# Optimization experiments

Measured on AMD Instinct MI355X. Metric: run time of the kernel, lower is better.

The kernel has to match this reference:

```python
import jax, jax.numpy as jnp
import numpy as np

B, L, IN, H, P, K, OUT = 16, 4096, 192, 512, 128, 6, 192  # P = ssm_size//2 (conj_sym)


def setup_inputs() -> dict:
    key = jax.random.key(0)
    ks = jax.random.split(key, 20)
    s = 1.0 / np.sqrt(H)
    inp = {
        'x': jax.random.normal(ks[0], (B, L, IN), jnp.float32),
        'W_enc': jax.random.normal(ks[1], (H, IN), jnp.float32) / np.sqrt(IN),
        'b_enc': jnp.zeros((H,), jnp.float32),
        'ln_scale': jnp.ones((K, H), jnp.float32),
        'ln_bias': jnp.zeros((K, H), jnp.float32),
        # HiPPO-like stable eigenvalues: negative real part
        'Lambda_re': -(0.5 * jax.random.uniform(ks[2], (K, P), jnp.float32) + 0.1),
        'Lambda_im': jnp.pi * jax.random.normal(ks[3], (K, P), jnp.float32),
        'B_re': jax.random.normal(ks[4], (K, P, H), jnp.float32) * s,
        'B_im': jax.random.normal(ks[5], (K, P, H), jnp.float32) * s,
        'C_re': jax.random.normal(ks[6], (K, H, P), jnp.float32) / np.sqrt(P),
        'C_im': jax.random.normal(ks[7], (K, H, P), jnp.float32) / np.sqrt(P),
        'D': jax.random.normal(ks[8], (K, H), jnp.float32),
        'log_step': jax.random.uniform(ks[9], (K, P), jnp.float32,
                                       minval=np.log(1e-3), maxval=np.log(1e-1)),
        'W_glu': jax.random.normal(ks[10], (K, H, H), jnp.float32) * s,
        'b_glu': jnp.zeros((K, H), jnp.float32),
        'W_dec': jax.random.normal(ks[11], (OUT, H), jnp.float32) * s,
        'b_dec': jnp.zeros((OUT,), jnp.float32),
    }
    return inp


def _layernorm(x, scale, bias, eps=1e-5):
    mu = jnp.mean(x, axis=-1, keepdims=True)
    var = jnp.var(x, axis=-1, keepdims=True)
    return (x - mu) * jax.lax.rsqrt(var + eps) * scale + bias


def _s5_ssm(u, lam_re, lam_im, b_re, b_im, c_re, c_im, d, log_step):
    # u: (L, H) real. Diagonal complex SSM, ZOH discretization, conj_sym output.
    lam = lam_re + 1j * lam_im                     # (P,)
    step = jnp.exp(log_step)                       # (P,) step_rescale = 1
    lam_bar = jnp.exp(lam * step)                  # (P,)
    Bm = b_re + 1j * b_im                          # (P, H)
    B_bar = ((lam_bar - 1.0) / lam)[:, None] * Bm  # ZOH input matrix
    Bu = u.astype(B_bar.dtype) @ B_bar.T           # (L, P) complex
    A = jnp.broadcast_to(lam_bar, Bu.shape)        # (L, P)

    def binop(e1, e2):
        a1, x1 = e1
        a2, x2 = e2
        return a2 * a1, a2 * x1 + x2

    _, xs = jax.lax.associative_scan(binop, (A, Bu))  # linear recurrence over L
    Cm = c_re + 1j * c_im                          # (H, P)
    y = 2.0 * jnp.real(xs @ Cm.T)                  # factor 2 from conjugate symmetry
    return y + u * d


def reference(x, W_enc, b_enc, ln_scale, ln_bias, Lambda_re, Lambda_im,
              B_re, B_im, C_re, C_im, D, log_step, W_glu, b_glu, W_dec, b_dec):
    def fwd_seq(xs):  # xs: (L, IN)
        h = xs @ W_enc.T + b_enc                   # encoder, vmapped over time
        for k in range(K):                         # stacked S5 blocks (prenorm)
            skip = h
            h = _layernorm(h, ln_scale[k], ln_bias[k])
            h = _s5_ssm(h, Lambda_re[k], Lambda_im[k], B_re[k], B_im[k],
                        C_re[k], C_im[k], D[k], log_step[k])
            h = jax.nn.gelu(h)
            h = h * jax.nn.sigmoid(h @ W_glu[k].T + b_glu[k])  # half-GLU
            h = skip + h
        return h @ W_dec.T + b_dec                 # decoder

    return jax.vmap(fwd_seq)(x)
```

## Files before the change

kernel.cpp:

```cpp
#include <hip/hip_runtime.h>
#include <math.h>

constexpr int  Bb   = 16;
constexpr int  Ll   = 4096;
constexpr int  INd  = 192;
constexpr int  Hd   = 512;
constexpr int  Kn   = 6;
constexpr int  OUTd = 192;
constexpr long Mrows = (long)Bb * Ll;

typedef _Float16 f16;
typedef _Float16 f16x8 __attribute__((ext_vector_type(8)));
typedef float    f32x4 __attribute__((ext_vector_type(4)));

__global__ void prep_lam_k(const float* __restrict__ Lre, const float* __restrict__ Lim,
                           const float* __restrict__ lstep,
                           float* lre, float* lim_, float* pre, float* pim,
                           float* cre, float* cim)
{
    int i = blockIdx.x * 256 + threadIdx.x;
    if (i >= Kn * 128) return;
    float lr = Lre[i], li = Lim[i];
    float st = expf(lstep[i]);
    float ar = lr * st, ai = li * st;
    float er = expf(ar);
    float sn, cs; sincosf(ai, &sn, &cs);
    float br = er * cs, bi = er * sn;
    lre[i] = br; lim_[i] = bi;
    float e2 = expf(64.f * ar);
    float sn2, cs2; sincosf(64.f * ai, &sn2, &cs2);
    pre[i] = e2 * cs2; pim[i] = e2 * sn2;
    float nr = br - 1.f, ni = bi;
    float den = lr * lr + li * li;
    cre[i] = (nr * lr + ni * li) / den;
    cim[i] = (ni * lr - nr * li) / den;
}

__global__ void prep_bbar_k(const float* __restrict__ Bre, const float* __restrict__ Bim,
                            const float* __restrict__ cre, const float* __restrict__ cim,
                            f16* __restrict__ Wh)
{
    int i = blockIdx.x * 256 + threadIdx.x;
    int h = i & 511;
    int p = (i >> 9) & 127;
    int k = i >> 16;
    float br = Bre[((size_t)(k * 128 + p)) * 512 + h];
    float bi = Bim[((size_t)(k * 128 + p)) * 512 + h];
    float cr = cre[k * 128 + p], ci = cim[k * 128 + p];
    Wh[(size_t)(k * 256 + p) * 512 + h]       = (f16)(cr * br - ci * bi);
    Wh[(size_t)(k * 256 + 128 + p) * 512 + h] = (f16)(cr * bi + ci * br);
}

__global__ void prep_c_k(const float* __restrict__ Cre, const float* __restrict__ Cim,
                         f16* __restrict__ Wh)
{
    int i = blockIdx.x * 256 + threadIdx.x;
    int p = i & 127;
    int h = (i >> 7) & 511;
    int k = i >> 16;
    float crv = Cre[((size_t)k * 512 + h) * 128 + p];
    float civ = Cim[((size_t)k * 512 + h) * 128 + p];
    size_t o = ((size_t)k * 512 + h) * 256;
    Wh[o + p]       = (f16)( 2.f * crv);
    Wh[o + 128 + p] = (f16)(-2.f * civ);
}

__global__ void cvt_w_k(const float* __restrict__ W, f16* __restrict__ Wh, long n)
{
    long i = (long)blockIdx.x * 256 + threadIdx.x;
    if (i >= n) return;
    Wh[i] = (f16)W[i];
}

__global__ __launch_bounds__(256)
void cvt_a_k(const float* __restrict__ in, f16* __restrict__ oh, long n8)
{
    long i = (long)blockIdx.x * 256 + threadIdx.x;
    if (i >= n8) return;
    const float* p = in + i * 8;
    float v[8];
    *(float4*)&v[0] = *(const float4*)p;
    *(float4*)&v[4] = *(const float4*)(p + 4);
    f16x8 vh;
#pragma unroll
    for (int j = 0; j < 8; ++j) vh[j] = (f16)v[j];
    *(f16x8*)(oh + i * 8) = vh;
}

__global__ __launch_bounds__(256)
void ln_k(const float* __restrict__ x, f16* __restrict__ oh,
          const float* __restrict__ sc, const float* __restrict__ bi)
{
    const int  lane = threadIdx.x & 63;
    const long row  = (long)blockIdx.x * 4 + (threadIdx.x >> 6);
    const float* p = x + row * 512 + lane * 8;
    float v[8];
    *(float4*)&v[0] = *(const float4*)p;
    *(float4*)&v[4] = *(const float4*)(p + 4);
    float s = 0.f;
#pragma unroll
    for (int j = 0; j < 8; ++j) s += v[j];
#pragma unroll
    for (int m = 1; m < 64; m <<= 1) s += __shfl_xor(s, m, 64);
    const float mu = s * (1.f / 512.f);
    float q = 0.f;
#pragma unroll
    for (int j = 0; j < 8; ++j) { float d = v[j] - mu; q += d * d; }
#pragma unroll
    for (int m = 1; m < 64; m <<= 1) q += __shfl_xor(q, m, 64);
    const float rs = rsqrtf(q * (1.f / 512.f) + 1e-5f);
    float sv[8], bv[8];
    *(float4*)&sv[0] = *(const float4*)(sc + lane * 8);
    *(float4*)&sv[4] = *(const float4*)(sc + lane * 8 + 4);
    *(float4*)&bv[0] = *(const float4*)(bi + lane * 8);
    *(float4*)&bv[4] = *(const float4*)(bi + lane * 8 + 4);
    f16x8 vh;
#pragma unroll
    for (int j = 0; j < 8; ++j)
        vh[j] = (f16)((v[j] - mu) * rs * sv[j] + bv[j]);
    *(f16x8*)(oh + row * 512 + lane * 8) = vh;
}

__global__ __launch_bounds__(256)
void scan_local_k(const float* __restrict__ Bu, float* __restrict__ fin,
                  const float* __restrict__ lre, const float* __restrict__ lim, int nB)
{
    const int g = blockIdx.x * 256 + threadIdx.x;
    const int p = g & 127;
    const int c = (g >> 7) & 63;
    const int b = g >> 13;
    if (b >= nB) return;
    const float ar = lre[p], ai = lim[p];
    const float* base = Bu + ((long)(b * Ll + c * 64)) * 256 + p;
    float xr = 0.f, xi = 0.f;
#pragma unroll 4
    for (int j = 0; j < 64; ++j) {
        float br  = base[j * 256];
        float bi2 = base[j * 256 + 128];
        float nr = fmaf(ar, xr, fmaf(-ai, xi, br));
        float ni = fmaf(ar, xi, fmaf( ai, xr, bi2));
        xr = nr; xi = ni;
    }
    long o = ((long)(b * 64 + c)) * 256 + p;
    fin[o] = xr; fin[o + 128] = xi;
}

__global__ void scan_carry_k(const float* __restrict__ fin, float* __restrict__ carry,
                             const float* __restrict__ pre, const float* __restrict__ pim,
                             int nB)
{
    const int g = blockIdx.x * 256 + threadIdx.x;
    if (g >= nB * 128) return;
    const int p = g & 127;
    const int b = g >> 7;
    const float pr = pre[p], pi = pim[p];
    float cr = 0.f, ci = 0.f;
    for (int c = 0; c < 64; ++c) {
        long o = ((long)(b * 64 + c)) * 256 + p;
        float fr = fin[o], fi = fin[o + 128];
        carry[o] = cr; carry[o + 128] = ci;
        float nr = fmaf(pr, cr, fmaf(-pi, ci, fr));
        float ni = fmaf(pr, ci, fmaf( pi, cr, fi));
        cr = nr; ci = ni;
    }
}

__global__ __launch_bounds__(256)
void scan_final_k(const float* __restrict__ Bu, const float* __restrict__ carry,
                  f16* __restrict__ xh,
                  const float* __restrict__ lre, const float* __restrict__ lim, int nB)
{
    const int g = blockIdx.x * 256 + threadIdx.x;
    const int p = g & 127;
    const int c = (g >> 7) & 63;
    const int b = g >> 13;
    if (b >= nB) return;
    const float ar = lre[p], ai = lim[p];
    long co = ((long)(b * 64 + c)) * 256 + p;
    float xr = carry[co], xi = carry[co + 128];
    const float* base = Bu + ((long)(b * Ll + c * 64)) * 256 + p;
    f16* bh = xh + ((long)(b * Ll + c * 64)) * 256 + p;
#pragma unroll 4
    for (int j = 0; j < 64; ++j) {
        float br  = base[j * 256];
        float bi2 = base[j * 256 + 128];
        float nr = fmaf(ar, xr, fmaf(-ai, xi, br));
        float ni = fmaf(ar, xi, fmaf( ai, xr, bi2));
        xr = nr; xi = ni;
        bh[j * 256]       = (f16)xr;
        bh[j * 256 + 128] = (f16)xi;
    }
}

template<int BN, int EPI>
__global__ __launch_bounds__(256)
void mgemm_k(const f16* __restrict__ A, const f16* __restrict__ Bw,
             float* __restrict__ C, int N, int Kd,
             const float* __restrict__ bias,
             const f16* __restrict__ aux, f16* __restrict__ outq)
{
    constexpr int BM = 128, BK = 32, LDA = 40;
    constexpr int FM = (BN == 128) ? 4 : 2;
    constexpr int WM = FM * 16;
    constexpr int FN = 4;
    __shared__ __align__(16) f16 As[BM][LDA];
    __shared__ __align__(16) f16 Bs[BN][LDA];

    const int tid  = threadIdx.x;
    const int wid  = tid >> 6;
    const int lane = tid & 63;
    const int l15  = lane & 15;
    const int l4   = lane >> 4;
    const int wm   = (BN == 128) ? (wid >> 1) : wid;
    const int wn   = (BN == 128) ? (wid & 1) : 0;

    const long bm = (long)blockIdx.y * BM;
    const int  bn = blockIdx.x * BN;

    f32x4 acc[FM][FN];
#pragma unroll
    for (int i = 0; i < FM; ++i)
#pragma unroll
        for (int j = 0; j < FN; ++j) acc[i][j] = (f32x4){0.f, 0.f, 0.f, 0.f};

    const int arow = tid >> 1;
    const int akc  = (tid & 1) * 16;
    const int brow = (BN == 128) ? (tid >> 1) : (tid >> 2);
    const int bko  = (BN == 128) ? ((tid & 1) * 16) : ((tid & 3) * 8);
    constexpr int NBL = (BN == 128) ? 2 : 1;

    f16x8 ra[2], rb[2];
    auto LOADT = [&](int k0) {
        const long aoff = (bm + arow) * (long)Kd + k0 + akc;
        ra[0] = *(const f16x8*)(A + aoff);
        ra[1] = *(const f16x8*)(A + aoff + 8);
        const long boff = (long)(bn + brow) * Kd + k0 + bko;
        rb[0] = *(const f16x8*)(Bw + boff);
        if constexpr (NBL == 2) rb[1] = *(const f16x8*)(Bw + boff + 8);
    };

    LOADT(0);
    for (int k0 = 0; k0 < Kd; k0 += BK) {
        __syncthreads();
        *(f16x8*)&As[arow][akc]     = ra[0];
        *(f16x8*)&As[arow][akc + 8] = ra[1];
        *(f16x8*)&Bs[brow][bko] = rb[0];
        if constexpr (NBL == 2) *(f16x8*)&Bs[brow][bko + 8] = rb[1];
        __syncthreads();
        if (k0 + BK < Kd) LOADT(k0 + BK);

        f16x8 bf[FN];
#pragma unroll
        for (int j = 0; j < FN; ++j)
            bf[j] = *(const f16x8*)&Bs[wn * 64 + j * 16 + l15][l4 * 8];
#pragma unroll
        for (int i = 0; i < FM; ++i) {
            f16x8 af = *(const f16x8*)&As[wm * WM + i * 16 + l15][l4 * 8];
#pragma unroll
            for (int j = 0; j < FN; ++j)
                acc[i][j] = __builtin_amdgcn_mfma_f32_16x16x32_f16(af, bf[j], acc[i][j], 0, 0, 0);
        }
    }

#pragma unroll
    for (int i = 0; i < FM; ++i)
#pragma unroll
        for (int j = 0; j < FN; ++j) {
            const int n = bn + wn * 64 + j * 16 + l15;
            float bv = 0.f;
            if constexpr (EPI != 0) bv = bias[n];
#pragma unroll
            for (int r = 0; r < 4; ++r) {
                const long m = bm + wm * WM + i * 16 + l4 * 4 + r;
                const long off = m * N + n;
                float v = acc[i][j][r];
                if constexpr (EPI == 0) {
                    C[off] = v;
                } else if constexpr (EPI == 1) {
                    C[off] = v + bv;
                } else if constexpr (EPI == 2) {
                    float y = v + (float)aux[off] * bv;
                    float t = tanhf(0.7978845608028654f * (y + 0.044715f * y * y * y));
                    outq[off] = (f16)(0.5f * y * (1.f + t));
                } else {
                    float z = v + bv;
                    C[off] += (float)aux[off] / (1.f + expf(-z));
                }
            }
        }
}

extern "C" void kernel_launch(void* const* d_in, const int* in_sizes, int n_in,
                              void* d_out, int out_size, void* d_ws, size_t ws_size,
                              hipStream_t stream)
{
    const float* x        = (const float*)d_in[0];
    const float* W_enc    = (const float*)d_in[1];
    const float* b_enc    = (const float*)d_in[2];
    const float* ln_scale = (const float*)d_in[3];
    const float* ln_bias  = (const float*)d_in[4];
    const float* Lre      = (const float*)d_in[5];
    const float* Lim      = (const float*)d_in[6];
    const float* B_re     = (const float*)d_in[7];
    const float* B_im     = (const float*)d_in[8];
    const float* C_re     = (const float*)d_in[9];
    const float* C_im     = (const float*)d_in[10];
    const float* Dv       = (const float*)d_in[11];
    const float* log_step = (const float*)d_in[12];
    const float* W_glu    = (const float*)d_in[13];
    const float* b_glu    = (const float*)d_in[14];
    const float* W_dec    = (const float*)d_in[15];
    const float* b_dec    = (const float*)d_in[16];
    float* out = (float*)d_out;

    char* w = (char*)d_ws;
    auto alloc = [&](size_t nbytes) { char* p = w; w += (nbytes + 255) & ~255ull; return p; };

    float* lam_re = (float*)alloc(768 * 4);
    float* lam_im = (float*)alloc(768 * 4);
    float* pow_re = (float*)alloc(768 * 4);
    float* pow_im = (float*)alloc(768 * 4);
    float* coef_re= (float*)alloc(768 * 4);
    float* coef_im= (float*)alloc(768 * 4);
    float* fin    = (float*)alloc((size_t)Bb * 64 * 256 * 4);
    float* carry  = (float*)alloc((size_t)Bb * 64 * 256 * 4);
    f16* WencH = (f16*)alloc((size_t)Hd * INd * 2);
    f16* WbuH  = (f16*)alloc((size_t)Kn * 256 * Hd * 2);
    f16* WcH   = (f16*)alloc((size_t)Kn * Hd * 256 * 2);
    f16* WgluH = (f16*)alloc((size_t)Kn * Hd * Hd * 2);
    f16* WdecH = (f16*)alloc((size_t)OUTd * Hd * 2);
    const size_t fixed_bytes = (size_t)(w - (char*)d_ws);

    int G = 1;
    for (; G < 16; G *= 2) {
        size_t Mg = Mrows / G;
        if (fixed_bytes + Mg * 4992ull <= ws_size) break;
    }
    const long Bg = Bb / G;
    const long Mg = Bg * Ll;

    float* h   = (float*)alloc((size_t)Mg * Hd * 4);
    f16*   uh  = (f16*)alloc((size_t)Mg * Hd * 2);
    float* Bu  = (float*)alloc((size_t)Mg * 256 * 4);
    f16*   xsh = (f16*)alloc((size_t)Mg * 256 * 2);
    f16*   xh  = (f16*)alloc((size_t)Mg * INd * 2);

    prep_lam_k <<<3,    256, 0, stream>>>(Lre, Lim, log_step, lam_re, lam_im,
                                          pow_re, pow_im, coef_re, coef_im);
    prep_bbar_k<<<1536, 256, 0, stream>>>(B_re, B_im, coef_re, coef_im, WbuH);
    prep_c_k   <<<1536, 256, 0, stream>>>(C_re, C_im, WcH);
    cvt_w_k    <<<6144, 256, 0, stream>>>(W_glu, WgluH, (long)Kn * Hd * Hd);
    cvt_w_k    <<<384,  256, 0, stream>>>(W_enc, WencH, (long)Hd * INd);
    cvt_w_k    <<<384,  256, 0, stream>>>(W_dec, WdecH, (long)OUTd * Hd);

    const dim3 blk(256);
    const int gy = (int)(Mg / 128);
    for (int g0 = 0; g0 < G; ++g0) {
        const float* xg   = x   + (size_t)g0 * Mg * INd;
        float*       outg = out + (size_t)g0 * Mg * OUTd;

        cvt_a_k<<<(int)(Mg * INd / 2048), 256, 0, stream>>>(xg, xh, Mg * INd / 8);
        mgemm_k<128, 1><<<dim3(4, gy), blk, 0, stream>>>(
            xh, WencH, h, 512, INd, b_enc, nullptr, nullptr);

        for (int k = 0; k < Kn; ++k) {
            ln_k<<<(int)(Mg / 4), 256, 0, stream>>>(h, uh,
                                                    ln_scale + k * 512, ln_bias + k * 512);
            mgemm_k<128, 0><<<dim3(2, gy), blk, 0, stream>>>(
                uh, WbuH + (size_t)k * 256 * Hd, Bu, 256, 512, nullptr, nullptr, nullptr);
            scan_local_k<<<(int)(Bg * 32), 256, 0, stream>>>(
                Bu, fin, lam_re + k * 128, lam_im + k * 128, (int)Bg);
            scan_carry_k<<<(int)((Bg * 128 + 255) / 256), 256, 0, stream>>>(
                fin, carry, pow_re + k * 128, pow_im + k * 128, (int)Bg);
            scan_final_k<<<(int)(Bg * 32), 256, 0, stream>>>(
                Bu, carry, xsh, lam_re + k * 128, lam_im + k * 128, (int)Bg);
            mgemm_k<128, 2><<<dim3(4, gy), blk, 0, stream>>>(
                xsh, WcH + (size_t)k * Hd * 256, nullptr, 512, 256,
                Dv + k * 512, uh, uh);
            mgemm_k<128, 3><<<dim3(4, gy), blk, 0, stream>>>(
                uh, WgluH + (size_t)k * Hd * Hd, h, 512, 512,
                b_glu + k * 512, uh, nullptr);
        }
        cvt_a_k<<<(int)(Mg * Hd / 2048), 256, 0, stream>>>(h, uh, Mg * Hd / 8);
        mgemm_k<64, 1><<<dim3(3, gy), blk, 0, stream>>>(
            uh, WdecH, outg, 192, 512, b_dec, nullptr, nullptr);
    }
}
```

Measured before the change: 2.471 ms.

## Fuse f32-to-f16 conversions into GEMMs, store Bu in fp16, parallelize carry scan

The encoder GEMM now reads fp32 input and converts it while loading, and the final GLU GEMM writes an fp16 copy of h for the decoder, which removes both standalone conversion kernels. Bu is stored as fp16 instead of fp32, halving the traffic for the two scan passes. The carry scan becomes a wave-level parallel prefix scan with shuffles instead of a serial loop over chunks. MFMA operands are swapped so each lane holds four consecutive columns, which lets the epilogues use vectorized 4-wide stores. Storing Bu in fp16 loses precision in the recurrence input.

```diff
diff --git a/kernel.cpp b/kernel.cpp
--- a/kernel.cpp
+++ b/kernel.cpp
@@ -11,6 +11,7 @@
 
 typedef _Float16 f16;
 typedef _Float16 f16x8 __attribute__((ext_vector_type(8)));
+typedef _Float16 f16x4 __attribute__((ext_vector_type(4)));
 typedef float    f32x4 __attribute__((ext_vector_type(4)));
 
 __global__ void prep_lam_k(const float* __restrict__ Lre, const float* __restrict__ Lim,
@@ -73,21 +74,6 @@
 }
 
 __global__ __launch_bounds__(256)
-void cvt_a_k(const float* __restrict__ in, f16* __restrict__ oh, long n8)
-{
-    long i = (long)blockIdx.x * 256 + threadIdx.x;
-    if (i >= n8) return;
-    const float* p = in + i * 8;
-    float v[8];
-    *(float4*)&v[0] = *(const float4*)p;
-    *(float4*)&v[4] = *(const float4*)(p + 4);
-    f16x8 vh;
-#pragma unroll
-    for (int j = 0; j < 8; ++j) vh[j] = (f16)v[j];
-    *(f16x8*)(oh + i * 8) = vh;
-}
-
-__global__ __launch_bounds__(256)
 void ln_k(const float* __restrict__ x, f16* __restrict__ oh,
           const float* __restrict__ sc, const float* __restrict__ bi)
 {
@@ -122,7 +108,7 @@
 }
 
 __global__ __launch_bounds__(256)
-void scan_local_k(const float* __restrict__ Bu, float* __restrict__ fin,
+void scan_local_k(const f16* __restrict__ Bu, float* __restrict__ fin,
                   const float* __restrict__ lre, const float* __restrict__ lim, int nB)
 {
     const int g = blockIdx.x * 256 + threadIdx.x;
@@ -131,12 +117,12 @@
     const int b = g >> 13;
     if (b >= nB) return;
     const float ar = lre[p], ai = lim[p];
-    const float* base = Bu + ((long)(b * Ll + c * 64)) * 256 + p;
+    const f16* base = Bu + ((long)(b * Ll + c * 64)) * 256 + p;
     float xr = 0.f, xi = 0.f;
 #pragma unroll 4
     for (int j = 0; j < 64; ++j) {
-        float br  = base[j * 256];
-        float bi2 = base[j * 256 + 128];
+        float br  = (float)base[j * 256];
+        float bi2 = (float)base[j * 256 + 128];
         float nr = fmaf(ar, xr, fmaf(-ai, xi, br));
         float ni = fmaf(ar, xi, fmaf( ai, xr, bi2));
         xr = nr; xi = ni;
@@ -145,28 +131,40 @@
     fin[o] = xr; fin[o + 128] = xi;
 }
 
-__global__ void scan_carry_k(const float* __restrict__ fin, float* __restrict__ carry,
-                             const float* __restrict__ pre, const float* __restrict__ pim,
-                             int nB)
-{
-    const int g = blockIdx.x * 256 + threadIdx.x;
-    if (g >= nB * 128) return;
-    const int p = g & 127;
-    const int b = g >> 7;
-    const float pr = pre[p], pi = pim[p];
-    float cr = 0.f, ci = 0.f;
-    for (int c = 0; c < 64; ++c) {
-        long o = ((long)(b * 64 + c)) * 256 + p;
-        float fr = fin[o], fi = fin[o + 128];
-        carry[o] = cr; carry[o + 128] = ci;
-        float nr = fmaf(pr, cr, fmaf(-pi, ci, fr));
-        float ni = fmaf(pr, ci, fmaf( pi, cr, fi));
-        cr = nr; ci = ni;
-    }
-}
-
 __global__ __launch_bounds__(256)
-void scan_final_k(const float* __restrict__ Bu, const float* __restrict__ carry,
+void scan_carry_k(const float* __restrict__ fin, float* __restrict__ carry,
+                  const float* __restrict__ pre, const float* __restrict__ pim, int nB)
+{
+    const int wv   = blockIdx.x * 4 + (threadIdx.x >> 6);
+    const int lane = threadIdx.x & 63;
+    if (wv >= nB * 128) return;
+    const int b = wv >> 7;
+    const int p = wv & 127;
+    const long o = ((long)(b * 64 + lane)) * 256 + p;
+    float xr = fin[o], xi = fin[o + 128];
+    float ar = pre[p], ai = pim[p];
+#pragma unroll
+    for (int s = 1; s < 64; s <<= 1) {
+        float par = __shfl_up(ar, s, 64);
+        float pai = __shfl_up(ai, s, 64);
+        float pxr = __shfl_up(xr, s, 64);
+        float pxi = __shfl_up(xi, s, 64);
+        if (lane >= s) {
+            float nxr = fmaf(ar, pxr, fmaf(-ai, pxi, xr));
+            float nxi = fmaf(ar, pxi, fmaf( ai, pxr, xi));
+            float nar = ar * par - ai * pai;
+            float nai = ar * pai + ai * par;
+            xr = nxr; xi = nxi; ar = nar; ai = nai;
+        }
+    }
+    float cr = __shfl_up(xr, 1, 64);
+    float ci = __shfl_up(xi, 1, 64);
+    if (lane == 0) { cr = 0.f; ci = 0.f; }
+    carry[o] = cr; carry[o + 128] = ci;
+}
+
+__global__ __launch_bounds__(256)
+void scan_final_k(const f16* __restrict__ Bu, const float* __restrict__ carry,
                   f16* __restrict__ xh,
                   const float* __restrict__ lre, const float* __restrict__ lim, int nB)
 {
@@ -178,12 +176,12 @@
     const float ar = lre[p], ai = lim[p];
     long co = ((long)(b * 64 + c)) * 256 + p;
     float xr = carry[co], xi = carry[co + 128];
-    const float* base = Bu + ((long)(b * Ll + c * 64)) * 256 + p;
+    const f16* base = Bu + ((long)(b * Ll + c * 64)) * 256 + p;
     f16* bh = xh + ((long)(b * Ll + c * 64)) * 256 + p;
 #pragma unroll 4
     for (int j = 0; j < 64; ++j) {
-        float br  = base[j * 256];
-        float bi2 = base[j * 256 + 128];
+        float br  = (float)base[j * 256];
+        float bi2 = (float)base[j * 256 + 128];
         float nr = fmaf(ar, xr, fmaf(-ai, xi, br));
         float ni = fmaf(ar, xi, fmaf( ai, xr, bi2));
         xr = nr; xi = ni;
@@ -192,9 +190,9 @@
     }
 }
 
-template<int BN, int EPI>
+template<int BN, int EPI, bool AF32>
 __global__ __launch_bounds__(256)
-void mgemm_k(const f16* __restrict__ A, const f16* __restrict__ Bw,
+void mgemm_k(const void* __restrict__ Ap, const f16* __restrict__ Bw,
              float* __restrict__ C, int N, int Kd,
              const float* __restrict__ bias,
              const f16* __restrict__ aux, f16* __restrict__ outq)
@@ -205,6 +203,9 @@
     constexpr int FN = 4;
     __shared__ __align__(16) f16 As[BM][LDA];
     __shared__ __align__(16) f16 Bs[BN][LDA];
+
+    const f16*   A16 = (const f16*)Ap;
+    const float* A32 = (const float*)Ap;
 
     const int tid  = threadIdx.x;
     const int wid  = tid >> 6;
@@ -231,9 +232,21 @@
 
     f16x8 ra[2], rb[2];
     auto LOADT = [&](int k0) {
-        const long aoff = (bm + arow) * (long)Kd + k0 + akc;
-        ra[0] = *(const f16x8*)(A + aoff);
-        ra[1] = *(const f16x8*)(A + aoff + 8);
+        if constexpr (AF32) {
+            const float* ap = A32 + (bm + arow) * (long)Kd + k0 + akc;
+            float4 t0 = ((const float4*)ap)[0];
+            float4 t1 = ((const float4*)ap)[1];
+            float4 t2 = ((const float4*)ap)[2];
+            float4 t3 = ((const float4*)ap)[3];
+            ra[0] = (f16x8){(f16)t0.x,(f16)t0.y,(f16)t0.z,(f16)t0.w,
+                            (f16)t1.x,(f16)t1.y,(f16)t1.z,(f16)t1.w};
+            ra[1] = (f16x8){(f16)t2.x,(f16)t2.y,(f16)t2.z,(f16)t2.w,
+                            (f16)t3.x,(f16)t3.y,(f16)t3.z,(f16)t3.w};
+        } else {
+            const long aoff = (bm + arow) * (long)Kd + k0 + akc;
+            ra[0] = *(const f16x8*)(A16 + aoff);
+            ra[1] = *(const f16x8*)(A16 + aoff + 8);
+        }
         const long boff = (long)(bn + brow) * Kd + k0 + bko;
         rb[0] = *(const f16x8*)(Bw + boff);
         if constexpr (NBL == 2) rb[1] = *(const f16x8*)(Bw + boff + 8);
@@ -258,36 +271,50 @@
             f16x8 af = *(const f16x8*)&As[wm * WM + i * 16 + l15][l4 * 8];
 #pragma unroll
             for (int j = 0; j < FN; ++j)
-                acc[i][j] = __builtin_amdgcn_mfma_f32_16x16x32_f16(af, bf[j], acc[i][j], 0, 0, 0);
+                acc[i][j] = __builtin_amdgcn_mfma_f32_16x16x32_f16(bf[j], af, acc[i][j], 0, 0, 0);
         }
     }
 
 #pragma unroll
-    for (int i = 0; i < FM; ++i)
+    for (int i = 0; i < FM; ++i) {
+        const int m = (int)(bm + wm * WM + i * 16 + l15);
 #pragma unroll
         for (int j = 0; j < FN; ++j) {
-            const int n = bn + wn * 64 + j * 16 + l15;
-            float bv = 0.f;
-            if constexpr (EPI != 0) bv = bias[n];
-#pragma unroll
-            for (int r = 0; r < 4; ++r) {
-                const long m = bm + wm * WM + i * 16 + l4 * 4 + r;
-                const long off = m * N + n;
-                float v = acc[i][j][r];
-                if constexpr (EPI == 0) {
-                    C[off] = v;
-                } else if constexpr (EPI == 1) {
-                    C[off] = v + bv;
-                } else if constexpr (EPI == 2) {
-                    float y = v + (float)aux[off] * bv;
+            const int  n0  = bn + wn * 64 + j * 16 + l4 * 4;
+            const long off = (long)m * N + n0;
+            f32x4 v = acc[i][j];
+            if constexpr (EPI == 0) {
+                *(f16x4*)(outq + off) = (f16x4){(f16)v[0], (f16)v[1], (f16)v[2], (f16)v[3]};
+            } else if constexpr (EPI == 1) {
+                const float4 bb = *(const float4*)(bias + n0);
+                *(float4*)(C + off) = make_float4(v[0]+bb.x, v[1]+bb.y, v[2]+bb.z, v[3]+bb.w);
+            } else if constexpr (EPI == 2) {
+                const float4 bb = *(const float4*)(bias + n0);
+                const f16x4 uu = *(const f16x4*)(aux + off);
+                f16x4 o4;
+#pragma unroll
+                for (int r = 0; r < 4; ++r) {
+                    float bvr = (r == 0 ? bb.x : r == 1 ? bb.y : r == 2 ? bb.z : bb.w);
+                    float y = v[r] + (float)uu[r] * bvr;
                     float t = tanhf(0.7978845608028654f * (y + 0.044715f * y * y * y));
-                    outq[off] = (f16)(0.5f * y * (1.f + t));
-                } else {
-                    float z = v + bv;
-                    C[off] += (float)aux[off] / (1.f + expf(-z));
+                    o4[r] = (f16)(0.5f * y * (1.f + t));
                 }
+                *(f16x4*)(outq + off) = o4;
+            } else {
+                const float4 bb = *(const float4*)(bias + n0);
+                const f16x4 uu = *(const f16x4*)(aux + off);
+                float4 hh = *(const float4*)(C + off);
+                float z0 = v[0]+bb.x, z1 = v[1]+bb.y, z2 = v[2]+bb.z, z3 = v[3]+bb.w;
+                hh.x += (float)uu[0] / (1.f + expf(-z0));
+                hh.y += (float)uu[1] / (1.f + expf(-z1));
+                hh.z += (float)uu[2] / (1.f + expf(-z2));
+                hh.w += (float)uu[3] / (1.f + expf(-z3));
+                *(float4*)(C + off) = hh;
+                if constexpr (EPI == 4)
+                    *(f16x4*)(outq + off) = (f16x4){(f16)hh.x, (f16)hh.y, (f16)hh.z, (f16)hh.w};
             }
         }
+    }
 }
 
 extern "C" void kernel_launch(void* const* d_in, const int* in_sizes, int n_in,
@@ -334,16 +361,15 @@
     int G = 1;
     for (; G < 16; G *= 2) {
         size_t Mg = Mrows / G;
-        if (fixed_bytes + Mg * 4992ull <= ws_size) break;
+        if (fixed_bytes + Mg * 4096ull <= ws_size) break;
     }
     const long Bg = Bb / G;
     const long Mg = Bg * Ll;
 
     float* h   = (float*)alloc((size_t)Mg * Hd * 4);
     f16*   uh  = (f16*)alloc((size_t)Mg * Hd * 2);
-    float* Bu  = (float*)alloc((size_t)Mg * 256 * 4);
+    f16*   Buh = (f16*)alloc((size_t)Mg * 256 * 2);
     f16*   xsh = (f16*)alloc((size_t)Mg * 256 * 2);
-    f16*   xh  = (f16*)alloc((size_t)Mg * INd * 2);
 
     prep_lam_k <<<3,    256, 0, stream>>>(Lre, Lim, log_step, lam_re, lam_im,
                                           pow_re, pow_im, coef_re, coef_im);
@@ -359,30 +385,33 @@
         const float* xg   = x   + (size_t)g0 * Mg * INd;
         float*       outg = out + (size_t)g0 * Mg * OUTd;
 
-        cvt_a_k<<<(int)(Mg * INd / 2048), 256, 0, stream>>>(xg, xh, Mg * INd / 8);
-        mgemm_k<128, 1><<<dim3(4, gy), blk, 0, stream>>>(
-            xh, WencH, h, 512, INd, b_enc, nullptr, nullptr);
+        mgemm_k<128, 1, true><<<dim3(4, gy), blk, 0, stream>>>(
+            xg, WencH, h, 512, INd, b_enc, nullptr, nullptr);
 
         for (int k = 0; k < Kn; ++k) {
             ln_k<<<(int)(Mg / 4), 256, 0, stream>>>(h, uh,
                                                     ln_scale + k * 512, ln_bias + k * 512);
-            mgemm_k<128, 0><<<dim3(2, gy), blk, 0, stream>>>(
-                uh, WbuH + (size_t)k * 256 * Hd, Bu, 256, 512, nullptr, nullptr, nullptr);
+            mgemm_k<128, 0, false><<<dim3(2, gy), blk, 0, stream>>>(
+                uh, WbuH + (size_t)k * 256 * Hd, nullptr, 256, 512, nullptr, nullptr, Buh);
             scan_local_k<<<(int)(Bg * 32), 256, 0, stream>>>(
-                Bu, fin, lam_re + k * 128, lam_im + k * 128, (int)Bg);
-            scan_carry_k<<<(int)((Bg * 128 + 255) / 256), 256, 0, stream>>>(
+                Buh, fin, lam_re + k * 128, lam_im + k * 128, (int)Bg);
+            scan_carry_k<<<(int)(Bg * 32), 256, 0, stream>>>(
                 fin, carry, pow_re + k * 128, pow_im + k * 128, (int)Bg);
             scan_final_k<<<(int)(Bg * 32), 256, 0, stream>>>(
-                Bu, carry, xsh, lam_re + k * 128, lam_im + k * 128, (int)Bg);
-            mgemm_k<128, 2><<<dim3(4, gy), blk, 0, stream>>>(
+                Buh, carry, xsh, lam_re + k * 128, lam_im + k * 128, (int)Bg);
+            mgemm_k<128, 2, false><<<dim3(4, gy), blk, 0, stream>>>(
                 xsh, WcH + (size_t)k * Hd * 256, nullptr, 512, 256,
                 Dv + k * 512, uh, uh);
-            mgemm_k<128, 3><<<dim3(4, gy), blk, 0, stream>>>(
-                uh, WgluH + (size_t)k * Hd * Hd, h, 512, 512,
-                b_glu + k * 512, uh, nullptr);
+            if (k < Kn - 1)
+                mgemm_k<128, 3, false><<<dim3(4, gy), blk, 0, stream>>>(
+                    uh, WgluH + (size_t)k * Hd * Hd, h, 512, 512,
+                    b_glu + k * 512, uh, nullptr);
+            else
+                mgemm_k<128, 4, false><<<dim3(4, gy), blk, 0, stream>>>(
+                    uh, WgluH + (size_t)k * Hd * Hd, h, 512, 512,
+                    b_glu + k * 512, uh, uh);
         }
-        cvt_a_k<<<(int)(Mg * Hd / 2048), 256, 0, stream>>>(h, uh, Mg * Hd / 8);
-        mgemm_k<64, 1><<<dim3(3, gy), blk, 0, stream>>>(
+        mgemm_k<64, 1, false><<<dim3(3, gy), blk, 0, stream>>>(
             uh, WdecH, outg, 192, 512, b_dec, nullptr, nullptr);
     }
 }
```

Measured after the change: 2.000 ms. -19.1%, faster.
